# Kernel optimization log

Measured on AMD Instinct MI355X. Metric: run time of the kernel, lower is better.

Reference implementation:

```python
import jax, jax.numpy as jnp
import numpy as np

EMA_OLD = 0.01  # original: m[z] = m[z]*0.01 + y*0.99
EMA_NEW = 0.99

def setup_inputs() -> dict:
    key = jax.random.key(0)
    k1, k2, k3, k4 = jax.random.split(key, 4)
    B, n, C, L = 4096, 1024, 64, 64
    y = jax.random.normal(k1, (B, C, L), dtype=jnp.float32)   # encoder latents
    m = jax.random.normal(k2, (n, C, L), dtype=jnp.float32)   # codebook means
    sd = jax.random.uniform(k3, (n, C, L), dtype=jnp.float32) # codebook variances (init ones in orig)
    p = jax.random.uniform(k4, (n,), dtype=jnp.float32)       # cluster counts
    return {"y": y, "m": m, "sd": sd, "p": p}

def reference(y, m, sd, p):
    B, C, L = y.shape
    n = m.shape[0]
    # pairwise squared distances via ||y||^2 - 2 y.m + ||m||^2 (GEMM form)
    yf = y.reshape(B, C * L)
    mf = m.reshape(n, C * L)
    d2 = ((yf * yf).sum(-1, keepdims=True)
          - 2.0 * (yf @ mf.T)
          + (mf * mf).sum(-1)[None, :])            # [B, n]
    z = jnp.argmin(d2, axis=1)                      # [B] assignments
    new_m = m.at[z].set(m[z] * EMA_OLD + y * EMA_NEW)
    # original updates sd using the ALREADY-updated m gathered at z
    mg = new_m[z]
    new_sd = sd.at[z].set((mg - y) ** 2 * EMA_OLD + sd[z] * EMA_NEW)
    return jnp.concatenate([new_m, new_sd], axis=0)  # [2n, C, L]
```

## Files before the change

### kernel.cpp

```cpp
#include <hip/hip_runtime.h>

#define B_ROWS 4096
#define N_CLUST 1024
#define KDIM 4096
#define NKT 32

#define EMA_OLD 0.01f
#define EMA_NEW 0.99f
#define MARGIN 2.0f

typedef unsigned short ushortT;
typedef _Float16 half8 __attribute__((ext_vector_type(8)));
typedef float f32x16 __attribute__((ext_vector_type(16)));

#define WS_WINNER_OFF 0
#define WS_Z_OFF      4096
#define WS_YY_OFF     20480
#define WS_MM_OFF     36864
#define WS_D2_OFF     65536
#define WS_YHI_OFF    (WS_D2_OFF + 16777216)
#define WS_MHI_OFF    (WS_YHI_OFF + 33554432)
#define WS_END        (WS_MHI_OFF + 8388608)

__global__ __launch_bounds__(256) void convert_sumsq(
    const float* __restrict__ ysrc, const float* __restrict__ msrc,
    ushortT* __restrict__ yhi, ushortT* __restrict__ mhi,
    float* __restrict__ yy, float* __restrict__ mm) {
    const int blk = blockIdx.x;
    const float* src;
    ushortT* hi;
    float* out;
    int row;
    if (blk < B_ROWS) {
        src = ysrc; hi = yhi; out = yy + blk; row = blk;
    } else {
        row = blk - B_ROWS;
        src = msrc; hi = mhi; out = mm + row;
    }
    const int r = row & 63, rb = row >> 6;
    const int t = threadIdx.x;
    float s = 0.f;
#pragma unroll
    for (int h = 0; h < 2; ++h) {
        int ci = h * 256 + t;
        int kt = ci >> 4, p = ci & 15;
        int c = p ^ (r & 15);
        const float* sp = src + ((size_t)row << 12) + kt * 128 + c * 8;
        float4 v0 = *(const float4*)sp;
        float4 v1 = *(const float4*)(sp + 4);
        float vv[8] = {v0.x, v0.y, v0.z, v0.w, v1.x, v1.y, v1.z, v1.w};
        half8 hv;
#pragma unroll
        for (int i = 0; i < 8; ++i) {
            hv[i] = (_Float16)vv[i];
            s += vv[i] * vv[i];
        }
        size_t off = (((size_t)rb * NKT + kt) * 64 + r) * 128 + p * 8;
        *(half8*)(hi + off) = hv;
    }
    for (int off = 32; off > 0; off >>= 1) s += __shfl_down(s, off, 64);
    __shared__ float red[4];
    if ((t & 63) == 0) red[t >> 6] = s;
    __syncthreads();
    if (t == 0) out[0] = red[0] + red[1] + red[2] + red[3];
}

__device__ __forceinline__ void gload_lds16(const void* g, void* l) {
    __builtin_amdgcn_global_load_lds(
        (const __attribute__((address_space(1))) unsigned int*)g,
        (__attribute__((address_space(3))) unsigned int*)l, 16, 0, 0);
}

__device__ __forceinline__ half8 ldfrag(const ushortT* s, int r, int c) {
    int p = c ^ (r & 15);
    return *(const half8*)(s + r * 128 + p * 8);
}

__global__ __launch_bounds__(256, 1) void screen_gemm(
    const ushortT* __restrict__ Ah, const ushortT* __restrict__ Bh,
    const float* __restrict__ yy, const float* __restrict__ mm,
    float* __restrict__ d2ws) {
    __shared__ __align__(16) ushortT sA[2][2 * 64 * 128];
    __shared__ __align__(16) ushortT sB[2][2 * 64 * 128];

    const int t = threadIdx.x, w = t >> 6, l = t & 63;
    const int bx = blockIdx.x >> 3, by = blockIdx.x & 7;
    const int row0 = bx * 128, col0 = by * 128;
    const int wr = (w >> 1) * 64, wc = (w & 1) * 64;
    const int m0 = l & 31, hsel = l >> 5;

    const char* gAbase = (const char*)Ah + (size_t)l * 16;
    const char* gBbase = (const char*)Bh + (size_t)l * 16;

    f32x16 acc[2][2];
#pragma unroll
    for (int i = 0; i < 2; ++i)
#pragma unroll
        for (int j = 0; j < 2; ++j)
#pragma unroll
            for (int r = 0; r < 16; ++r) acc[i][j][r] = 0.f;

#define STAGE(buf, kt)                                                        \
    {                                                                         \
        _Pragma("unroll")                                                     \
        for (int j = 0; j < 8; ++j) {                                         \
            int ch = w * 8 + j;                                               \
            int tile = ch >> 4, seg = ch & 15;                                \
            size_t go = ((size_t)((2 * bx + tile) * NKT + (kt)) << 14) +      \
                        seg * 1024;                                           \
            gload_lds16(gAbase + go,                                          \
                        (char*)&sA[buf][0] + tile * 16384 + seg * 1024);      \
            size_t gob = ((size_t)((2 * by + tile) * NKT + (kt)) << 14) +     \
                         seg * 1024;                                          \
            gload_lds16(gBbase + gob,                                         \
                        (char*)&sB[buf][0] + tile * 16384 + seg * 1024);      \
        }                                                                     \
    }

    STAGE(0, 0);

    for (int kt = 0; kt < NKT; ++kt) {
        const int buf = kt & 1;
        if (kt + 1 < NKT) {
            STAGE(buf ^ 1, kt + 1);
            asm volatile("s_waitcnt vmcnt(16)" ::: "memory");
        } else {
            asm volatile("s_waitcnt vmcnt(0)" ::: "memory");
        }
        __builtin_amdgcn_s_barrier();

        const ushortT* tA = &sA[buf][(wr >> 6) * 8192];
        const ushortT* tB = &sB[buf][(wc >> 6) * 8192];
#pragma unroll
        for (int kk = 0; kk < 8; ++kk) {
            int c = kk * 2 + hsel;
            half8 a0 = ldfrag(tA, m0, c);
            half8 a1 = ldfrag(tA, 32 + m0, c);
            half8 b0 = ldfrag(tB, m0, c);
            half8 b1 = ldfrag(tB, 32 + m0, c);
            acc[0][0] = __builtin_amdgcn_mfma_f32_32x32x16_f16(a0, b0, acc[0][0], 0, 0, 0);
            acc[0][1] = __builtin_amdgcn_mfma_f32_32x32x16_f16(a0, b1, acc[0][1], 0, 0, 0);
            acc[1][0] = __builtin_amdgcn_mfma_f32_32x32x16_f16(a1, b0, acc[1][0], 0, 0, 0);
            acc[1][1] = __builtin_amdgcn_mfma_f32_32x32x16_f16(a1, b1, acc[1][1], 0, 0, 0);
        }
        asm volatile("" ::: "memory");
        __builtin_amdgcn_s_barrier();
    }
#undef STAGE

#pragma unroll
    for (int i = 0; i < 2; ++i)
#pragma unroll
        for (int j = 0; j < 2; ++j) {
            const int gcol = col0 + wc + j * 32 + m0;
            const float mv = mm[gcol];
#pragma unroll
            for (int r = 0; r < 16; ++r) {
                int ri = (r & 3) + 8 * (r >> 2) + 4 * hsel;
                int grow = row0 + wr + i * 32 + ri;
                d2ws[(size_t)grow * N_CLUST + gcol] =
                    yy[grow] - 2.0f * acc[i][j][r] + mv;
            }
        }
}

__global__ __launch_bounds__(256) void rescreen(
    const float* __restrict__ d2ws, const float* __restrict__ ysrc,
    const float* __restrict__ msrc, const float* __restrict__ yy,
    const float* __restrict__ mm, int* __restrict__ z) {
    const int row = blockIdx.x * 4 + (threadIdx.x >> 6);
    const int l = threadIdx.x & 63;
    const float* dr = d2ws + (size_t)row * N_CLUST;

    float v[16];
#pragma unroll
    for (int k = 0; k < 16; ++k) v[k] = dr[l + 64 * k];

    float mn = v[0];
#pragma unroll
    for (int k = 1; k < 16; ++k) mn = fminf(mn, v[k]);
#pragma unroll
    for (int s = 1; s <= 32; s <<= 1) mn = fminf(mn, __shfl_xor(mn, s, 64));
    const float thr = mn + MARGIN;

    int cnt = 0;
#pragma unroll
    for (int k = 0; k < 16; ++k) cnt += (v[k] <= thr) ? 1 : 0;
#pragma unroll
    for (int s = 1; s <= 32; s <<= 1) cnt += __shfl_xor(cnt, s, 64);

    int zj;
    if (cnt == 1) {
        int cj = 0x7FFFFFFF;
#pragma unroll
        for (int k = 0; k < 16; ++k)
            if (v[k] <= thr) cj = min(cj, l + 64 * k);
#pragma unroll
        for (int s = 1; s <= 32; s <<= 1) cj = min(cj, __shfl_xor(cj, s, 64));
        zj = cj;
    } else {
        double bestd = 1e300;
        int bestj = -1;
        const float4* yp = (const float4*)(ysrc + (size_t)row * KDIM);
        for (int k = 0; k < 16; ++k) {
            unsigned long long mask = __ballot(v[k] <= thr);
            while (mask) {
                int lb = __ffsll((unsigned long long)mask) - 1;
                mask &= mask - 1;
                int j = 64 * k + lb;
                const float4* mp = (const float4*)(msrc + (size_t)j * KDIM);
                double acc = 0.0;
#pragma unroll
                for (int tt = 0; tt < 16; ++tt) {
                    float4 a = yp[l + 64 * tt];
                    float4 b = mp[l + 64 * tt];
                    acc += (double)a.x * b.x + (double)a.y * b.y +
                           (double)a.z * b.z + (double)a.w * b.w;
                }
#pragma unroll
                for (int s = 1; s <= 32; s <<= 1)
                    acc += __shfl_xor(acc, s, 64);
                double d2x = (double)yy[row] - 2.0 * acc + (double)mm[j];
                if (d2x < bestd) { bestd = d2x; bestj = j; }
            }
        }
        zj = bestj;
    }
    if (l == 0) z[row] = zj;
}

__global__ void pick_winner(const int* __restrict__ z,
                            int* __restrict__ winner) {
    int b = blockIdx.x * blockDim.x + threadIdx.x;
    if (b < B_ROWS) atomicMax(&winner[z[b]], b);
}

__global__ __launch_bounds__(256) void write_out(
    const float* __restrict__ y, const float* __restrict__ m,
    const float* __restrict__ sd, const int* __restrict__ winner,
    float* __restrict__ out) {
    const int idx = blockIdx.x;
    const int t = threadIdx.x;
    const int w = winner[idx];
    const float4* mp = (const float4*)(m + (size_t)idx * KDIM);
    const float4* sp = (const float4*)(sd + (size_t)idx * KDIM);
    float4* om = (float4*)(out + (size_t)idx * KDIM);
    float4* os = (float4*)(out + (size_t)(N_CLUST + idx) * KDIM);
    if (w >= 0) {
        const float4* yp = (const float4*)(y + (size_t)w * KDIM);
        for (int i = t; i < KDIM / 4; i += 256) {
            float4 mv = mp[i], yv = yp[i], sv = sp[i];
            float4 nm, ns;
            nm.x = mv.x * EMA_OLD + yv.x * EMA_NEW;
            nm.y = mv.y * EMA_OLD + yv.y * EMA_NEW;
            nm.z = mv.z * EMA_OLD + yv.z * EMA_NEW;
            nm.w = mv.w * EMA_OLD + yv.w * EMA_NEW;
            float dx = nm.x - yv.x, dy = nm.y - yv.y;
            float dz = nm.z - yv.z, dw = nm.w - yv.w;
            ns.x = dx * dx * EMA_OLD + sv.x * EMA_NEW;
            ns.y = dy * dy * EMA_OLD + sv.y * EMA_NEW;
            ns.z = dz * dz * EMA_OLD + sv.z * EMA_NEW;
            ns.w = dw * dw * EMA_OLD + sv.w * EMA_NEW;
            om[i] = nm;
            os[i] = ns;
        }
    } else {
        for (int i = t; i < KDIM / 4; i += 256) {
            om[i] = mp[i];
            os[i] = sp[i];
        }
    }
}

extern "C" void kernel_launch(void* const* d_in, const int* in_sizes, int n_in,
                              void* d_out, int out_size, void* d_ws,
                              size_t ws_size, hipStream_t stream) {
    const float* y  = (const float*)d_in[0];
    const float* m  = (const float*)d_in[1];
    const float* sd = (const float*)d_in[2];
    float* out = (float*)d_out;

    char* ws = (char*)d_ws;
    int* winner = (int*)(ws + WS_WINNER_OFF);
    int* z      = (int*)(ws + WS_Z_OFF);
    float* yy   = (float*)(ws + WS_YY_OFF);
    float* mm   = (float*)(ws + WS_MM_OFF);
    float* d2ws = (float*)(ws + WS_D2_OFF);
    ushortT* yhi = (ushortT*)(ws + WS_YHI_OFF);
    ushortT* mhi = (ushortT*)(ws + WS_MHI_OFF);

    hipMemsetAsync(winner, 0xFF, 4096, stream);

    convert_sumsq<<<B_ROWS + N_CLUST, 256, 0, stream>>>(y, m, yhi, mhi, yy, mm);

    screen_gemm<<<(B_ROWS / 128) * (N_CLUST / 128), 256, 0, stream>>>(
        yhi, mhi, yy, mm, d2ws);

    rescreen<<<B_ROWS / 4, 256, 0, stream>>>(d2ws, y, m, yy, mm, z);

    pick_winner<<<B_ROWS / 256, 256, 0, stream>>>(z, winner);
    write_out<<<N_CLUST, 256, 0, stream>>>(y, m, sd, winner, out);
}
```

Baseline: 229.7 us.

## Split screening GEMM K dimension in two and single-buffer LDS for occupancy

The screening GEMM now splits the K reduction across two blocks, doubling the grid from 256 to 512 blocks. Each half writes a partial distance matrix, and rescreen adds the two partials as it reads them. LDS double-buffering is dropped for a single buffer, and launch bounds allow two blocks per CU. This targets the low occupancy of 256 blocks on a GPU with many CUs. In exchange it writes and reads an extra 16 MB partial buffer and loses the overlap between loads and MFMA within a block.

```diff
diff --git a/kernel.cpp b/kernel.cpp
--- a/kernel.cpp
+++ b/kernel.cpp
@@ -17,8 +17,9 @@
 #define WS_Z_OFF      4096
 #define WS_YY_OFF     20480
 #define WS_MM_OFF     36864
-#define WS_D2_OFF     65536
-#define WS_YHI_OFF    (WS_D2_OFF + 16777216)
+#define WS_D2A_OFF    65536
+#define WS_D2B_OFF    (WS_D2A_OFF + 16777216)
+#define WS_YHI_OFF    (WS_D2B_OFF + 16777216)
 #define WS_MHI_OFF    (WS_YHI_OFF + 33554432)
 #define WS_END        (WS_MHI_OFF + 8388608)
 
@@ -76,15 +77,17 @@
     return *(const half8*)(s + r * 128 + p * 8);
 }
 
-__global__ __launch_bounds__(256, 1) void screen_gemm(
+__global__ __launch_bounds__(256, 2) void screen_gemm(
     const ushortT* __restrict__ Ah, const ushortT* __restrict__ Bh,
     const float* __restrict__ yy, const float* __restrict__ mm,
-    float* __restrict__ d2ws) {
-    __shared__ __align__(16) ushortT sA[2][2 * 64 * 128];
-    __shared__ __align__(16) ushortT sB[2][2 * 64 * 128];
+    float* __restrict__ d2a, float* __restrict__ d2b) {
+    __shared__ __align__(16) ushortT sA[128 * 128];
+    __shared__ __align__(16) ushortT sB[128 * 128];
 
     const int t = threadIdx.x, w = t >> 6, l = t & 63;
-    const int bx = blockIdx.x >> 3, by = blockIdx.x & 7;
+    const int by = blockIdx.x & 7;
+    const int kh = (blockIdx.x >> 3) & 1;
+    const int bx = blockIdx.x >> 4;
     const int row0 = bx * 128, col0 = by * 128;
     const int wr = (w >> 1) * 64, wc = (w & 1) * 64;
     const int m0 = l & 31, hsel = l >> 5;
@@ -100,37 +103,25 @@
 #pragma unroll
             for (int r = 0; r < 16; ++r) acc[i][j][r] = 0.f;
 
-#define STAGE(buf, kt)                                                        \
-    {                                                                         \
-        _Pragma("unroll")                                                     \
-        for (int j = 0; j < 8; ++j) {                                         \
-            int ch = w * 8 + j;                                               \
-            int tile = ch >> 4, seg = ch & 15;                                \
-            size_t go = ((size_t)((2 * bx + tile) * NKT + (kt)) << 14) +      \
-                        seg * 1024;                                           \
-            gload_lds16(gAbase + go,                                          \
-                        (char*)&sA[buf][0] + tile * 16384 + seg * 1024);      \
-            size_t gob = ((size_t)((2 * by + tile) * NKT + (kt)) << 14) +     \
-                         seg * 1024;                                          \
-            gload_lds16(gBbase + gob,                                         \
-                        (char*)&sB[buf][0] + tile * 16384 + seg * 1024);      \
-        }                                                                     \
-    }
-
-    STAGE(0, 0);
-
-    for (int kt = 0; kt < NKT; ++kt) {
-        const int buf = kt & 1;
-        if (kt + 1 < NKT) {
-            STAGE(buf ^ 1, kt + 1);
-            asm volatile("s_waitcnt vmcnt(16)" ::: "memory");
-        } else {
-            asm volatile("s_waitcnt vmcnt(0)" ::: "memory");
-        }
-        __builtin_amdgcn_s_barrier();
-
-        const ushortT* tA = &sA[buf][(wr >> 6) * 8192];
-        const ushortT* tB = &sB[buf][(wc >> 6) * 8192];
+    const int kt0 = kh * (NKT / 2);
+    for (int ktt = 0; ktt < NKT / 2; ++ktt) {
+        const int kt = kt0 + ktt;
+        __syncthreads();
+#pragma unroll
+        for (int j = 0; j < 8; ++j) {
+            int ch = w * 8 + j;
+            int tile = ch >> 4, seg = ch & 15;
+            size_t go = ((size_t)((2 * bx + tile) * NKT + kt) << 14) +
+                        seg * 1024;
+            gload_lds16(gAbase + go, (char*)sA + tile * 16384 + seg * 1024);
+            size_t gob = ((size_t)((2 * by + tile) * NKT + kt) << 14) +
+                         seg * 1024;
+            gload_lds16(gBbase + gob, (char*)sB + tile * 16384 + seg * 1024);
+        }
+        __syncthreads();
+
+        const ushortT* tA = sA + (wr >> 6) * 8192;
+        const ushortT* tB = sB + (wc >> 6) * 8192;
 #pragma unroll
         for (int kk = 0; kk < 8; ++kk) {
             int c = kk * 2 + hsel;
@@ -143,38 +134,52 @@
             acc[1][0] = __builtin_amdgcn_mfma_f32_32x32x16_f16(a1, b0, acc[1][0], 0, 0, 0);
             acc[1][1] = __builtin_amdgcn_mfma_f32_32x32x16_f16(a1, b1, acc[1][1], 0, 0, 0);
         }
-        asm volatile("" ::: "memory");
-        __builtin_amdgcn_s_barrier();
-    }
-#undef STAGE
-
-#pragma unroll
-    for (int i = 0; i < 2; ++i)
-#pragma unroll
-        for (int j = 0; j < 2; ++j) {
-            const int gcol = col0 + wc + j * 32 + m0;
-            const float mv = mm[gcol];
-#pragma unroll
-            for (int r = 0; r < 16; ++r) {
-                int ri = (r & 3) + 8 * (r >> 2) + 4 * hsel;
-                int grow = row0 + wr + i * 32 + ri;
-                d2ws[(size_t)grow * N_CLUST + gcol] =
-                    yy[grow] - 2.0f * acc[i][j][r] + mv;
+    }
+
+    if (kh == 0) {
+#pragma unroll
+        for (int i = 0; i < 2; ++i)
+#pragma unroll
+            for (int j = 0; j < 2; ++j) {
+                const int gcol = col0 + wc + j * 32 + m0;
+                const float mv = mm[gcol];
+#pragma unroll
+                for (int r = 0; r < 16; ++r) {
+                    int ri = (r & 3) + 8 * (r >> 2) + 4 * hsel;
+                    int grow = row0 + wr + i * 32 + ri;
+                    d2a[(size_t)grow * N_CLUST + gcol] =
+                        yy[grow] - 2.0f * acc[i][j][r] + mv;
+                }
             }
-        }
+    } else {
+#pragma unroll
+        for (int i = 0; i < 2; ++i)
+#pragma unroll
+            for (int j = 0; j < 2; ++j) {
+                const int gcol = col0 + wc + j * 32 + m0;
+#pragma unroll
+                for (int r = 0; r < 16; ++r) {
+                    int ri = (r & 3) + 8 * (r >> 2) + 4 * hsel;
+                    int grow = row0 + wr + i * 32 + ri;
+                    d2b[(size_t)grow * N_CLUST + gcol] = -2.0f * acc[i][j][r];
+                }
+            }
+    }
 }
 
 __global__ __launch_bounds__(256) void rescreen(
-    const float* __restrict__ d2ws, const float* __restrict__ ysrc,
-    const float* __restrict__ msrc, const float* __restrict__ yy,
-    const float* __restrict__ mm, int* __restrict__ z) {
+    const float* __restrict__ d2a, const float* __restrict__ d2b,
+    const float* __restrict__ ysrc, const float* __restrict__ msrc,
+    const float* __restrict__ yy, const float* __restrict__ mm,
+    int* __restrict__ z) {
     const int row = blockIdx.x * 4 + (threadIdx.x >> 6);
     const int l = threadIdx.x & 63;
-    const float* dr = d2ws + (size_t)row * N_CLUST;
+    const float* dra = d2a + (size_t)row * N_CLUST;
+    const float* drb = d2b + (size_t)row * N_CLUST;
 
     float v[16];
 #pragma unroll
-    for (int k = 0; k < 16; ++k) v[k] = dr[l + 64 * k];
+    for (int k = 0; k < 16; ++k) v[k] = dra[l + 64 * k] + drb[l + 64 * k];
 
     float mn = v[0];
 #pragma unroll
@@ -285,7 +290,8 @@
     int* z      = (int*)(ws + WS_Z_OFF);
     float* yy   = (float*)(ws + WS_YY_OFF);
     float* mm   = (float*)(ws + WS_MM_OFF);
-    float* d2ws = (float*)(ws + WS_D2_OFF);
+    float* d2a  = (float*)(ws + WS_D2A_OFF);
+    float* d2b  = (float*)(ws + WS_D2B_OFF);
     ushortT* yhi = (ushortT*)(ws + WS_YHI_OFF);
     ushortT* mhi = (ushortT*)(ws + WS_MHI_OFF);
 
@@ -293,10 +299,10 @@
 
     convert_sumsq<<<B_ROWS + N_CLUST, 256, 0, stream>>>(y, m, yhi, mhi, yy, mm);
 
-    screen_gemm<<<(B_ROWS / 128) * (N_CLUST / 128), 256, 0, stream>>>(
-        yhi, mhi, yy, mm, d2ws);
-
-    rescreen<<<B_ROWS / 4, 256, 0, stream>>>(d2ws, y, m, yy, mm, z);
+    screen_gemm<<<(B_ROWS / 128) * (N_CLUST / 128) * 2, 256, 0, stream>>>(
+        yhi, mhi, yy, mm, d2a, d2b);
+
+    rescreen<<<B_ROWS / 4, 256, 0, stream>>>(d2a, d2b, y, m, yy, mm, z);
 
     pick_winner<<<B_ROWS / 256, 256, 0, stream>>>(z, winner);
     write_out<<<N_CLUST, 256, 0, stream>>>(y, m, sd, winner, out);
```

After: 216.3 us. 5.8% less time.
